# Optimization experiments

Hardware: AMD Instinct MI355X
Metric: run time of the kernel (lower is better)

Reference implementation:

```python
import jax, jax.numpy as jnp
import numpy as np

EPS = 1e-5
HEADS = 8
GROUPS = 8
DIM_HEAD = 64
SCALE = DIM_HEAD ** -0.5
DSF = 4            # downsample_factor
OFF_SCALE = 4.0    # offset_scale
OFF_PAD = 1        # (offset_kernel_size - downsample_factor)//2


def batchnorm(x, g, b):
    # training-mode BatchNorm2d: biased batch stats over (N,H,W)
    m = x.mean(axis=(0, 2, 3), keepdims=True)
    v = x.var(axis=(0, 2, 3), keepdims=True)
    return (x - m) * jax.lax.rsqrt(v + EPS) * g[None, :, None, None] + b[None, :, None, None]


def grouped_conv1x1(x, w):
    # x: (B, G*Ci, H, W), w: (G, Co, Ci) -> (B, G*Co, H, W)
    B, C, H, W = x.shape
    G, Co, Ci = w.shape
    y = jnp.einsum('bgchw,goc->bgohw', x.reshape(B, G, Ci, H, W), w)
    return y.reshape(B, G * Co, H, W)


def conv1x1(x, w, b):
    # x: (B,C,H,W), w: (O,C), b: (O,)
    return jnp.einsum('bchw,oc->bohw', x, w) + b[None, :, None, None]


def norm_grid(h, w):
    # (h,w,2) with channel order (x,y); matches lucidrains create_grid_like+normalize_grid
    # (original normalizes x by h-1, y by w-1; identical for square maps)
    gy, gx = jnp.meshgrid(jnp.arange(h, dtype=jnp.float32), jnp.arange(w, dtype=jnp.float32), indexing='ij')
    nx = 2.0 * gx / max(h - 1, 1) - 1.0
    ny = 2.0 * gy / max(w - 1, 1) - 1.0
    return jnp.stack([nx, ny], axis=-1)


def grid_sample_bilinear(img, grid):
    # img: (N,C,H,W); grid: (N,Hg,Wg,2) with (x,y) in [-1,1]
    # mode='bilinear', padding_mode='zeros', align_corners=False (torch F.grid_sample)
    N, C, H, W = img.shape
    x = ((grid[..., 0] + 1.0) * W - 1.0) * 0.5
    y = ((grid[..., 1] + 1.0) * H - 1.0) * 0.5
    x0 = jnp.floor(x)
    y0 = jnp.floor(y)
    wx1 = x - x0
    wy1 = y - y0
    x0i = x0.astype(jnp.int32)
    y0i = y0.astype(jnp.int32)

    def gather(ix, iy):
        valid = (ix >= 0) & (ix < W) & (iy >= 0) & (iy < H)
        ixc = jnp.clip(ix, 0, W - 1)
        iyc = jnp.clip(iy, 0, H - 1)
        vals = jax.vmap(lambda im, yy, xx: im[:, yy, xx])(img, iyc, ixc)  # (N,C,Hg,Wg)
        return vals * valid[:, None, :, :].astype(img.dtype)

    v00 = gather(x0i, y0i)
    v10 = gather(x0i + 1, y0i)
    v01 = gather(x0i, y0i + 1)
    v11 = gather(x0i + 1, y0i + 1)
    wx1e = wx1[:, None]
    wy1e = wy1[:, None]
    return (v00 * (1 - wx1e) * (1 - wy1e) + v10 * wx1e * (1 - wy1e)
            + v01 * (1 - wx1e) * wy1e + v11 * wx1e * wy1e)


def deformable_attention(x, q_w, k_w, v_w, off_dw_w, off_dw_b, off_pw_w,
                         cpb_w0, cpb_b0, cpb_w1, cpb_b1, cpb_w2, cpb_b2,
                         out_w, out_b):
    B, C, H, W = x.shape
    G = GROUPS
    Cg = C // G  # offset_dims = 64

    q = grouped_conv1x1(x, q_w)  # (B,C,H,W)

    # offsets from grouped queries: depthwise 6x6 stride-4 conv -> GELU -> 1x1 -> tanh*scale
    gq = q.reshape(B * G, Cg, H, W)
    off = jax.lax.conv_general_dilated(
        gq, off_dw_w, window_strides=(DSF, DSF), padding=[(OFF_PAD, OFF_PAD)] * 2,
        feature_group_count=Cg, dimension_numbers=('NCHW', 'OIHW', 'NCHW'))
    off = off + off_dw_b[None, :, None, None]
    off = jax.nn.gelu(off, approximate=False)
    off = jnp.einsum('bchw,oc->bohw', off, off_pw_w)  # (BG,2,h2,w2)
    off = jnp.tanh(off) * OFF_SCALE
    h2, w2 = off.shape[-2:]

    # vgrid = integer grid + offsets, normalized to [-1,1] (channel order x,y)
    gy, gx = jnp.meshgrid(jnp.arange(h2, dtype=x.dtype), jnp.arange(w2, dtype=x.dtype), indexing='ij')
    vgrid = jnp.stack([gx, gy], axis=0)[None] + off  # (BG,2,h2,w2)
    vx = 2.0 * vgrid[:, 0] / max(h2 - 1, 1) - 1.0
    vy = 2.0 * vgrid[:, 1] / max(w2 - 1, 1) - 1.0
    vgrid_scaled = jnp.stack([vx, vy], axis=-1)  # (BG,h2,w2,2)

    # sample kv features at deformed locations
    kv = grid_sample_bilinear(x.reshape(B * G, Cg, H, W), vgrid_scaled)
    kv = kv.reshape(B, C, h2, w2)
    k = grouped_conv1x1(kv, k_w)
    v = grouped_conv1x1(kv, v_w)

    q = q * SCALE

    def to_heads(t):
        b, c, hh, ww = t.shape
        return t.reshape(b, HEADS, DIM_HEAD, hh * ww).transpose(0, 1, 3, 2)  # b h (hw) d

    qh, kh, vh = to_heads(q), to_heads(k), to_heads(v)
    sim = jnp.einsum('bhid,bhjd->bhij', qh, kh)  # (B,H,i=HW,j=h2*w2)

    # continuous positional bias (CPB)
    i, j = H * W, h2 * w2
    grid_q = norm_grid(H, W).reshape(i, 2)
    grid_kv = vgrid_scaled.reshape(B * G, j, 2)
    pos = grid_q[None, :, None, :] - grid_kv[:, None, :, :]  # (BG,i,j,2)
    bias = jnp.sign(pos) * jnp.log(jnp.abs(pos) + 1.0)
    bias = jax.nn.relu(bias @ cpb_w0 + cpb_b0)
    bias = jax.nn.relu(bias @ cpb_w1 + cpb_b1)
    bias = bias @ cpb_w2 + cpb_b2  # (BG,i,j,o) with o = heads//groups = 1
    o = HEADS // G
    bias = bias.reshape(B, G, i, j, o).transpose(0, 1, 4, 2, 3).reshape(B, G * o, i, j)

    attn = jax.nn.softmax(sim + bias, axis=-1)  # (max-subtract in original == stable softmax)
    out = jnp.einsum('bhij,bhjd->bhid', attn, vh)
    out = out.transpose(0, 1, 3, 2).reshape(B, HEADS * DIM_HEAD, H, W)
    return conv1x1(out, out_w, out_b)


def setup_inputs() -> dict:
    key = jax.random.key(0)
    ks = jax.random.split(key, 12)
    B, C, H, W = 2, 512, 32, 32
    G = GROUPS
    s = 0.02
    f32 = jnp.float32
    return {
        'x': jax.random.normal(ks[0], (B, C, H, W), f32),
        'n1_g': jnp.ones((C,), f32), 'n1_b': jnp.zeros((C,), f32),
        'n2_g': jnp.ones((C,), f32), 'n2_b': jnp.zeros((C,), f32),
        'q_w': jax.random.normal(ks[1], (G, C // G, C // G), f32) * s,
        'k_w': jax.random.normal(ks[2], (G, C // G, C // G), f32) * s,
        'v_w': jax.random.normal(ks[3], (G, C // G, C // G), f32) * s,
        'off_dw_w': jax.random.normal(ks[4], (C // G, 1, 6, 6), f32) * s,
        'off_dw_b': jnp.zeros((C // G,), f32),
        'off_pw_w': jax.random.normal(ks[5], (2, C // G), f32) * s,
        'cpb_w0': jax.random.normal(ks[6], (2, 128), f32) * s, 'cpb_b0': jnp.zeros((128,), f32),
        'cpb_w1': jax.random.normal(ks[7], (128, 128), f32) * s, 'cpb_b1': jnp.zeros((128,), f32),
        'cpb_w2': jax.random.normal(ks[8], (128, 1), f32) * s, 'cpb_b2': jnp.zeros((1,), f32),
        'out_w': jax.random.normal(ks[9], (C, C), f32) * s, 'out_b': jnp.zeros((C,), f32),
        'mlp_w1': jax.random.normal(ks[10], (4 * C, C), f32) * s, 'mlp_b1': jnp.zeros((4 * C,), f32),
        'mlp_w2': jax.random.normal(ks[11], (C, 4 * C), f32) * s, 'mlp_b2': jnp.zeros((C,), f32),
    }


def reference(x, n1_g, n1_b, n2_g, n2_b, q_w, k_w, v_w, off_dw_w, off_dw_b, off_pw_w,
              cpb_w0, cpb_b0, cpb_w1, cpb_b1, cpb_w2, cpb_b2, out_w, out_b,
              mlp_w1, mlp_b1, mlp_w2, mlp_b2):
    x = x + deformable_attention(batchnorm(x, n1_g, n1_b), q_w, k_w, v_w,
                                 off_dw_w, off_dw_b, off_pw_w,
                                 cpb_w0, cpb_b0, cpb_w1, cpb_b1, cpb_w2, cpb_b2,
                                 out_w, out_b)
    h = batchnorm(x, n2_g, n2_b)
    h = jax.nn.gelu(conv1x1(h, mlp_w1, mlp_b1), approximate=False)
    h = conv1x1(h, mlp_w2, mlp_b2)
    return x + h
```

## Files before the change

### kernel.cpp

```cpp
#include <hip/hip_runtime.h>
#include <cstdint>
#include <cstddef>

#define BATCH 2
#define CCH   512
#define HWPIX 1024
#define SCALE 0.125f
#define TU0  (-1.45f)
#define TDU  (2.9f/63.0f)
#define TINV (63.0f/2.9f)

typedef short bh8 __attribute__((ext_vector_type(8)));
typedef float f32x4 __attribute__((ext_vector_type(4)));
typedef unsigned short u16;
typedef u16 us8 __attribute__((ext_vector_type(8)));
typedef u16 us4 __attribute__((ext_vector_type(4)));

__device__ __forceinline__ u16 f2bf(float f){
  unsigned u = __float_as_uint(f);
  unsigned r = (u + 0x7FFFu + ((u>>16)&1u))>>16;
  return (u16)r;
}
__device__ __forceinline__ float geluf(float v){ return 0.5f*v*(1.0f + erff(v*0.70710678118654752f)); }

__global__ __launch_bounds__(256) void prep_kernel(
    const float* __restrict__ qw, const float* __restrict__ kw, const float* __restrict__ vw,
    const float* __restrict__ ow, const float* __restrict__ m1, const float* __restrict__ m2,
    u16* __restrict__ wdst,
    const float* __restrict__ x, const float* __restrict__ g, const float* __restrict__ bta,
    float* __restrict__ AB,
    const float* __restrict__ w0, const float* __restrict__ b0,
    const float* __restrict__ w1, const float* __restrict__ b1,
    const float* __restrict__ w2, const float* __restrict__ b2,
    float* __restrict__ tab){
  __shared__ float ls[4], lss[4];
  __shared__ float red[16][17];
  __shared__ __align__(16) float w1s[4096];
  __shared__ float h0s[16*33];
  int blk = blockIdx.x; int t = threadIdx.x;
  if(blk < 2400){
    int idx = (blk*256 + t)*4;
    if(idx >= 2457600) return;
    const float* src; int off;
    if(idx < 32768){ src=qw; off=idx; }
    else if(idx <   65536){ src=kw; off=idx-32768; }
    else if(idx <   98304){ src=vw; off=idx-65536; }
    else if(idx <  360448){ src=ow; off=idx-98304; }
    else if(idx < 1409024){ src=m1; off=idx-360448; }
    else                  { src=m2; off=idx-1409024; }
    float4 v = *(const float4*)&src[off];
    *(us4*)&wdst[idx] = (us4){f2bf(v.x), f2bf(v.y), f2bf(v.z), f2bf(v.w)};
  } else if(blk < 2912){
    int c = blk - 2400;
    float s=0.f, ss=0.f;
    for(int b=0;b<BATCH;b++){
      size_t base = (size_t)b*CCH*HWPIX + (size_t)c*HWPIX;
      for(int p=t;p<HWPIX;p+=256){
        float v = x[base+p];
        s += v; ss += v*v;
      }
    }
    for(int o=32;o;o>>=1){ s += __shfl_down(s,o); ss += __shfl_down(ss,o); }
    int w = t>>6, lane = t&63;
    if(lane==0){ ls[w]=s; lss[w]=ss; }
    __syncthreads();
    if(t==0){
      float S=ls[0]+ls[1]+ls[2]+ls[3], SS=lss[0]+lss[1]+lss[2]+lss[3];
      float m = S*(1.0f/2048.0f);
      float var = SS*(1.0f/2048.0f) - m*m;
      float r = rsqrtf(var + 1e-5f);
      AB[c]     = r*g[c];
      AB[512+c] = bta[c] - m*r*g[c];
    }
  } else {
    int eloc = t & 15, chunk = t >> 4;
    int eb = (blk-2912)*16;
    int e = eb + eloc;
    float acc[8] = {0.f,0.f,0.f,0.f,0.f,0.f,0.f,0.f};
    for(int kc=0;kc<128;kc+=32){
      #pragma unroll
      for(int r=0;r<4;r++){
        int idx = r*1024 + t*4;
        *(f32x4*)&w1s[idx] = *(const f32x4*)&w1[kc*128 + idx];
      }
      #pragma unroll
      for(int j=0;j<2;j++){
        int job = j*256 + t;
        int el = job & 15, kk = job >> 4;
        int ee = eb + el;
        float uu = TU0 + (float)(ee&63)*TDU;
        float vv = TU0 + (float)(ee>>6)*TDU;
        int k = kc + kk;
        h0s[el*33 + kk] = fmaxf(fmaf(uu, w0[k], fmaf(vv, w0[128+k], b0[k])), 0.f);
      }
      __syncthreads();
      #pragma unroll 8
      for(int kk=0;kk<32;kk++){
        float h = h0s[eloc*33 + kk];
        const float* wr = &w1s[kk*128 + chunk*8];
        #pragma unroll
        for(int n=0;n<8;n++) acc[n] = fmaf(h, wr[n], acc[n]);
      }
      __syncthreads();
    }
    float partial = 0.f;
    #pragma unroll
    for(int n=0;n<8;n++)
      partial = fmaf(fmaxf(acc[n] + b1[chunk*8+n], 0.f), w2[chunk*8+n], partial);
    red[eloc][chunk] = partial;
    __syncthreads();
    if(chunk==0){
      float s = b2[0];
      #pragma unroll
      for(int c2=0;c2<16;c2++) s += red[eloc][c2];
      tab[e] = s;
    }
  }
}

__global__ __launch_bounds__(256) void bnstat_kernel(const float* __restrict__ src,
      const float* __restrict__ g, const float* __restrict__ bta, float* __restrict__ AB){
  int c = blockIdx.x; int t = threadIdx.x;
  float s=0.f, ss=0.f;
  for(int b=0;b<BATCH;b++){
    size_t base = (size_t)b*CCH*HWPIX + (size_t)c*HWPIX;
    for(int p=t;p<HWPIX;p+=256){
      float v = src[base+p];
      s += v; ss += v*v;
    }
  }
  for(int o=32;o;o>>=1){ s += __shfl_down(s,o); ss += __shfl_down(ss,o); }
  __shared__ float ls[4], lss[4];
  int w = t>>6, lane = t&63;
  if(lane==0){ ls[w]=s; lss[w]=ss; }
  __syncthreads();
  if(t==0){
    float S=ls[0]+ls[1]+ls[2]+ls[3], SS=lss[0]+lss[1]+lss[2]+lss[3];
    float m = S*(1.0f/2048.0f);
    float var = SS*(1.0f/2048.0f) - m*m;
    float r = rsqrtf(var + 1e-5f);
    AB[c]     = r*g[c];
    AB[512+c] = bta[c] - m*r*g[c];
  }
}

__global__ __launch_bounds__(256) void bntrans_kernel(const float* __restrict__ src,
      const float* __restrict__ AB, float* __restrict__ dstF, u16* __restrict__ dstT, int tMode){
  __shared__ float tile[64*65];
  int t = threadIdx.x;
  int p0 = blockIdx.x*64, gq = blockIdx.y, b = blockIdx.z;
  int pl = t&63, seg = t>>6;
  #pragma unroll
  for(int r=0;r<16;r++){
    int c = seg*16 + r;
    int ch = gq*64 + c;
    size_t a = (size_t)b*524288 + (size_t)ch*1024 + p0 + pl;
    float v = src[a]*AB[ch] + AB[512+ch];
    tile[c*65 + pl] = v;
    if(dstF) dstF[a] = v;
  }
  __syncthreads();
  int c = t&63;
  #pragma unroll
  for(int r=0;r<16;r++){
    int p = seg*16 + r;
    float v = tile[c*65 + p];
    size_t a = tMode ? ((size_t)b*524288 + (size_t)(p0+p)*512 + gq*64 + c)
                     : ((size_t)(b*8+gq)*65536 + (size_t)(p0+p)*64 + c);
    dstT[a] = f2bf(v);
  }
}

template<int NT, int TOUT>
__global__ __launch_bounds__(256,4) void gemm_lds(
    const u16* __restrict__ W, const u16* __restrict__ Xt,
    float* __restrict__ outF, u16* __restrict__ outT,
    const float* __restrict__ bias, const float* __restrict__ resF,
    int M, int K, int Nb, int wMask, int wStride, int doGelu){
  __shared__ __align__(16) u16 xS[64*NT*64];
  __shared__ __align__(16) u16 wS[64*64];
  int t = threadIdx.x;
  int w = t>>6, lane = t&63, l15 = lane&15, quad = lane>>4;
  int n0 = blockIdx.x*(64*NT), m0 = blockIdx.y*64, batch = blockIdx.z;
  const u16* Wg = W + (size_t)(batch & wMask)*wStride + (size_t)m0*K;
  const u16* Xg = Xt + (size_t)batch*Nb*K + (size_t)n0*K;
  const u16* pX[2*NT]; u16* sX[2*NT];
  #pragma unroll
  for(int p=0;p<2*NT;p++){
    int row = (p*256 + t)>>3, kb = t&7;
    pX[p] = Xg + (size_t)row*K + kb*8;
    sX[p] = &xS[(row*8 + (kb ^ (row&7)))*8];
  }
  int row0 = t>>3,        kb0 = t&7;
  int row1 = (256+t)>>3,  kb1 = t&7;
  const u16* pW0 = Wg + (size_t)row0*K + kb0*8;
  const u16* pW1 = Wg + (size_t)row1*K + kb1*8;
  u16* sW0 = &wS[(row0*8 + (kb0 ^ (row0&7)))*8];
  u16* sW1 = &wS[(row1*8 + (kb1 ^ (row1&7)))*8];
  f32x4 acc[4][NT];
  #pragma unroll
  for(int mt=0;mt<4;mt++)
    #pragma unroll
    for(int nt=0;nt<NT;nt++) acc[mt][nt] = (f32x4){0.f,0.f,0.f,0.f};
  us8 rx[2*NT], rw0, rw1;
  #pragma unroll
  for(int p=0;p<2*NT;p++) rx[p] = *(const us8*)pX[p];
  rw0 = *(const us8*)pW0; rw1 = *(const us8*)pW1;
  for(int kc=0;kc<K;kc+=64){
    #pragma unroll
    for(int p=0;p<2*NT;p++) *(us8*)sX[p] = rx[p];
    *(us8*)sW0 = rw0;  *(us8*)sW1 = rw1;
    __syncthreads();
    if(kc+64 < K){
      #pragma unroll
      for(int p=0;p<2*NT;p++) rx[p] = *(const us8*)(pX[p] + kc+64);
      rw0 = *(const us8*)(pW0 + kc+64);  rw1 = *(const us8*)(pW1 + kc+64);
    }
    #pragma unroll
    for(int ks=0;ks<2;ks++){
      bh8 bF[NT];
      #pragma unroll
      for(int nt=0;nt<NT;nt++){
        int rb = (w*NT + nt)*16 + l15;
        bF[nt] = *(const bh8*)&xS[rb*64 + ((ks*4+quad) ^ (rb&7))*8];
      }
      #pragma unroll
      for(int mt=0;mt<4;mt++){
        int ra = mt*16 + l15;
        bh8 aF = *(const bh8*)&wS[ra*64 + ((ks*4+quad) ^ (ra&7))*8];
        #pragma unroll
        for(int nt=0;nt<NT;nt++)
          acc[mt][nt] = __builtin_amdgcn_mfma_f32_16x16x32_bf16(aF, bF[nt], acc[mt][nt], 0,0,0);
      }
    }
    __syncthreads();
  }
  if(TOUT==1){
    size_t oB = (size_t)batch*Nb*(size_t)M;
    #pragma unroll
    for(int nt=0;nt<NT;nt++){
      int n = n0 + (w*NT + nt)*16 + l15;
      #pragma unroll
      for(int mt=0;mt<4;mt++){
        int m = m0 + mt*16 + quad*4;
        us4 pk;
        #pragma unroll
        for(int reg=0;reg<4;reg++){
          float v = acc[mt][nt][reg];
          if(bias) v += bias[m+reg];
          if(doGelu) v = geluf(v);
          pk[reg] = f2bf(v);
        }
        *(us4*)&outT[oB + (size_t)n*M + m] = pk;
      }
    }
  } else if(TOUT==2){
    size_t oBF = (size_t)batch*(size_t)M*Nb;
    size_t oBT = (size_t)batch*Nb*(size_t)M;
    #pragma unroll
    for(int nt=0;nt<NT;nt++){
      int n = n0 + (w*NT + nt)*16 + l15;
      #pragma unroll
      for(int mt=0;mt<4;mt++){
        int m = m0 + mt*16 + quad*4;
        us4 pk;
        #pragma unroll
        for(int reg=0;reg<4;reg++){
          float v = acc[mt][nt][reg];
          outF[oBF + (size_t)(m+reg)*Nb + n] = v;
          pk[reg] = f2bf(v*SCALE);
        }
        *(us4*)&outT[oBT + (size_t)n*M + m] = pk;
      }
    }
  } else {
    size_t oB = (size_t)batch*(size_t)M*Nb;
    #pragma unroll
    for(int nt=0;nt<NT;nt++){
      int n = n0 + (w*NT + nt)*16 + l15;
      #pragma unroll
      for(int mt=0;mt<4;mt++)
        #pragma unroll
        for(int reg=0;reg<4;reg++){
          int m = m0 + mt*16 + quad*4 + reg;
          float v = acc[mt][nt][reg];
          if(bias) v += bias[m];
          if(doGelu) v = geluf(v);
          size_t a = oB + (size_t)m*Nb + n;
          if(resF) v += resF[a];
          outF[a] = v;
        }
    }
  }
}

__global__ __launch_bounds__(256) void dwconv_kernel(const float* __restrict__ q,
    const float* __restrict__ dw, const float* __restrict__ dwb, float* __restrict__ offg){
  int t = threadIdx.x;
  int bgc = blockIdx.x*4 + (t>>6);
  int c = bgc & 63;
  int pix = t&63;
  int oy = pix>>3, ox = pix&7;
  const float* img = q + (size_t)bgc*HWPIX;
  float acc = dwb[c];
  #pragma unroll
  for(int ky=0;ky<6;ky++){
    int y = oy*4 - 1 + ky;
    if(y<0 || y>31) continue;
    #pragma unroll
    for(int kx=0;kx<6;kx++){
      int x = ox*4 - 1 + kx;
      if(x<0 || x>31) continue;
      acc = fmaf(img[y*32 + x], dw[c*36 + ky*6 + kx], acc);
    }
  }
  offg[(size_t)bgc*64 + pix] = geluf(acc);
}

__device__ __forceinline__ float fetchpix(const float* img, int ix, int iy){
  return (ix>=0 && ix<32 && iy>=0 && iy<32) ? img[iy*32+ix] : 0.0f;
}
__global__ __launch_bounds__(256) void samplekv_kernel(
    const float* __restrict__ xn, const float* __restrict__ offg, const float* __restrict__ pw,
    const u16* __restrict__ kwb, const u16* __restrict__ vwb,
    float* __restrict__ vgrid, u16* __restrict__ kTb, float* __restrict__ vbuf){
  __shared__ __align__(16) u16 kvS[64*64];
  __shared__ float redA[64][5], redB[64][5];
  __shared__ float sVG[128];
  int bg = blockIdx.x; int t = threadIdx.x;
  int p = t&63, cq = t>>6;
  float a0=0.f, a1=0.f;
  for(int c=cq*16;c<cq*16+16;c++){
    float v = offg[(size_t)bg*4096 + c*64 + p];
    a0 = fmaf(v, pw[c], a0);
    a1 = fmaf(v, pw[64+c], a1);
  }
  redA[p][cq] = a0; redB[p][cq] = a1;
  __syncthreads();
  if(t < 64){
    float s0 = redA[t][0]+redA[t][1]+redA[t][2]+redA[t][3];
    float s1 = redB[t][0]+redB[t][1]+redB[t][2]+redB[t][3];
    float o0 = tanhf(s0)*4.0f, o1 = tanhf(s1)*4.0f;
    float gx = (float)(t&7), gy = (float)(t>>3);
    float vxx = (2.0f/7.0f)*(gx + o0) - 1.0f;
    float vyy = (2.0f/7.0f)*(gy + o1) - 1.0f;
    sVG[t*2]   = vxx;  sVG[t*2+1] = vyy;
    vgrid[bg*128 + t*2]   = vxx;
    vgrid[bg*128 + t*2+1] = vyy;
  }
  __syncthreads();
  {
    float vx = sVG[p*2], vy = sVG[p*2+1];
    float xs = ((vx + 1.0f)*32.0f - 1.0f)*0.5f;
    float ys = ((vy + 1.0f)*32.0f - 1.0f)*0.5f;
    float x0 = floorf(xs), y0 = floorf(ys);
    float wx = xs - x0, wy = ys - y0;
    int ix0 = (int)x0, iy0 = (int)y0;
    int b = bg>>3, g = bg&7;
    float w00 = (1.f-wx)*(1.f-wy), w10 = wx*(1.f-wy), w01 = (1.f-wx)*wy, w11 = wx*wy;
    u16 tmp[16];
    #pragma unroll
    for(int cc=0;cc<16;cc++){
      int c = cq*16 + cc;
      const float* img = xn + (size_t)b*CCH*HWPIX + (size_t)(g*64+c)*HWPIX;
      float acc = w00*fetchpix(img,ix0,iy0)   + w10*fetchpix(img,ix0+1,iy0)
                + w01*fetchpix(img,ix0,iy0+1) + w11*fetchpix(img,ix0+1,iy0+1);
      tmp[cc] = f2bf(acc);
    }
    int kb0 = cq*2, kb1 = cq*2+1;
    *(us8*)&kvS[p*64 + ((kb0 ^ (p&7))<<3)] = *(us8*)&tmp[0];
    *(us8*)&kvS[p*64 + ((kb1 ^ (p&7))<<3)] = *(us8*)&tmp[8];
  }
  __syncthreads();
  int w = t>>6, lane = t&63, l15 = lane&15, quad = lane>>4;
  int g8 = bg&7;
  const u16* kW = kwb + (size_t)g8*4096 + quad*8;
  const u16* vW = vwb + (size_t)g8*4096 + quad*8;
  int rb = w*16 + l15;
  bh8 bF[2];
  #pragma unroll
  for(int ks=0;ks<2;ks++)
    bF[ks] = *(const bh8*)&kvS[rb*64 + ((ks*4+quad) ^ (rb&7))*8];
  {
    f32x4 acc[4];
    #pragma unroll
    for(int mt=0;mt<4;mt++) acc[mt] = (f32x4){0.f,0.f,0.f,0.f};
    #pragma unroll
    for(int ks=0;ks<2;ks++)
      #pragma unroll
      for(int mt=0;mt<4;mt++){
        bh8 aF = *(const bh8*)&kW[(size_t)(mt*16+l15)*64 + ks*32];
        acc[mt] = __builtin_amdgcn_mfma_f32_16x16x32_bf16(aF, bF[ks], acc[mt], 0,0,0);
      }
    int n = w*16 + l15;
    #pragma unroll
    for(int mt=0;mt<4;mt++){
      us4 pk;
      #pragma unroll
      for(int reg=0;reg<4;reg++) pk[reg] = f2bf(acc[mt][reg]);
      *(us4*)&kTb[(size_t)bg*4096 + (size_t)n*64 + mt*16 + quad*4] = pk;
    }
  }
  {
    f32x4 acc[4];
    #pragma unroll
    for(int mt=0;mt<4;mt++) acc[mt] = (f32x4){0.f,0.f,0.f,0.f};
    #pragma unroll
    for(int ks=0;ks<2;ks++)
      #pragma unroll
      for(int mt=0;mt<4;mt++){
        bh8 aF = *(const bh8*)&vW[(size_t)(mt*16+l15)*64 + ks*32];
        acc[mt] = __builtin_amdgcn_mfma_f32_16x16x32_bf16(aF, bF[ks], acc[mt], 0,0,0);
      }
    int n = w*16 + l15;
    #pragma unroll
    for(int mt=0;mt<4;mt++)
      #pragma unroll
      for(int reg=0;reg<4;reg++)
        vbuf[(size_t)bg*4096 + (size_t)(mt*16 + quad*4 + reg)*64 + n] = acc[mt][reg];
  }
}

__global__ __launch_bounds__(256) void biaseval_kernel(
    const float* __restrict__ vgrid, const float* __restrict__ tab,
    float* __restrict__ biasOut){
  int t = threadIdx.x;
  int bg = blockIdx.x >> 6, jj = blockIdx.x & 63;
  float vx = vgrid[bg*128 + jj*2];
  float vy = vgrid[bg*128 + jj*2 + 1];
  int i0 = t*4;
  int gy = i0 >> 5, gx0 = i0 & 31;
  float py = (2.0f/31.0f)*(float)gy - 1.0f - vy;
  float v = copysignf(__logf(1.0f + fabsf(py)), py);
  float fv = (v - TU0) * TINV;
  int iv = (int)floorf(fv);
  iv = iv < 0 ? 0 : (iv > 62 ? 62 : iv);
  fv -= (float)iv;
  f32x4 res;
  #pragma unroll
  for(int c=0;c<4;c++){
    float px = (2.0f/31.0f)*(float)(gx0 + c) - 1.0f - vx;
    float u = copysignf(__logf(1.0f + fabsf(px)), px);
    float fu = (u - TU0) * TINV;
    int iu = (int)floorf(fu);
    iu = iu < 0 ? 0 : (iu > 62 ? 62 : iu);
    fu -= (float)iu;
    const float* p0 = &tab[iv*64 + iu];
    const float* p1 = p0 + 64;
    float a = fmaf(fu, p0[1] - p0[0], p0[0]);
    float b = fmaf(fu, p1[1] - p1[0], p1[0]);
    res[c] = fmaf(fv, b - a, a);
  }
  *(f32x4*)&biasOut[(size_t)bg*65536 + (size_t)jj*1024 + i0] = res;
}

__global__ __launch_bounds__(256) void attn_kernel(
    const u16* __restrict__ qTb, const u16* __restrict__ kTb, const float* __restrict__ vb,
    const float* __restrict__ biasb, u16* __restrict__ obT){
  __shared__ __align__(16) u16 qS[64*64], kS[64*64];
  __shared__ __align__(16) u16 vS[64*72], pS[64*72];
  int t = threadIdx.x;
  int w = t>>6, lane = t&63, l15 = lane&15, quad = lane>>4;
  int bg = blockIdx.x>>4, itile = blockIdx.x&15;
  int i0 = itile*64;
  #pragma unroll
  for(int p=0;p<2;p++){
    int idx = p*256 + t;
    int row = idx>>3, kb = t&7;
    int sw = ((kb ^ (row&7)))*8;
    *(us8*)&qS[row*64 + sw] = *(const us8*)&qTb[(size_t)bg*65536 + (size_t)(i0+row)*64 + kb*8];
    *(us8*)&kS[row*64 + sw] = *(const us8*)&kTb[(size_t)bg*4096  + (size_t)row*64      + kb*8];
  }
  for(int e=t;e<4096;e+=256){
    int d = e>>6, j = e&63;
    vS[d*72 + j] = f2bf(vb[(size_t)bg*4096 + e]);
  }
  __syncthreads();
  f32x4 sAcc[4];
  #pragma unroll
  for(int jt=0;jt<4;jt++){
    int jg = jt*16 + l15;
    sAcc[jt] = *(const f32x4*)&biasb[(size_t)bg*65536 + (size_t)jg*1024 + i0 + w*16 + quad*4];
  }
  int ra = w*16 + l15;
  #pragma unroll
  for(int ks=0;ks<2;ks++){
    bh8 aF = *(const bh8*)&qS[ra*64 + ((ks*4+quad) ^ (ra&7))*8];
    #pragma unroll
    for(int jt=0;jt<4;jt++){
      int rb = jt*16 + l15;
      bh8 bF = *(const bh8*)&kS[rb*64 + ((ks*4+quad) ^ (rb&7))*8];
      sAcc[jt] = __builtin_amdgcn_mfma_f32_16x16x32_bf16(aF, bF, sAcc[jt], 0,0,0);
    }
  }
  #pragma unroll
  for(int reg=0;reg<4;reg++){
    float m = fmaxf(fmaxf(sAcc[0][reg], sAcc[1][reg]), fmaxf(sAcc[2][reg], sAcc[3][reg]));
    m = fmaxf(m, __shfl_xor(m, 1));
    m = fmaxf(m, __shfl_xor(m, 2));
    m = fmaxf(m, __shfl_xor(m, 4));
    m = fmaxf(m, __shfl_xor(m, 8));
    float li = 0.f;
    #pragma unroll
    for(int jt=0;jt<4;jt++){
      float e = __expf(sAcc[jt][reg] - m);
      sAcc[jt][reg] = e;
      li += e;
    }
    li += __shfl_xor(li, 1);
    li += __shfl_xor(li, 2);
    li += __shfl_xor(li, 4);
    li += __shfl_xor(li, 8);
    float inv = 1.0f / li;
    #pragma unroll
    for(int jt=0;jt<4;jt++) sAcc[jt][reg] *= inv;
  }
  #pragma unroll
  for(int jt=0;jt<4;jt++)
    #pragma unroll
    for(int reg=0;reg<4;reg++)
      pS[(w*16 + quad*4 + reg)*72 + jt*16 + l15] = f2bf(sAcc[jt][reg]);
  __syncthreads();
  f32x4 oAcc[4];
  #pragma unroll
  for(int dt=0;dt<4;dt++) oAcc[dt] = (f32x4){0.f,0.f,0.f,0.f};
  int rp = w*16 + l15;
  #pragma unroll
  for(int ks=0;ks<2;ks++){
    bh8 aP = *(const bh8*)&pS[rp*72 + ks*32 + quad*8];
    #pragma unroll
    for(int dt=0;dt<4;dt++){
      bh8 bV = *(const bh8*)&vS[(dt*16 + l15)*72 + ks*32 + quad*8];
      oAcc[dt] = __builtin_amdgcn_mfma_f32_16x16x32_bf16(aP, bV, oAcc[dt], 0,0,0);
    }
  }
  int b = bg>>3, g = bg&7;
  #pragma unroll
  for(int dt=0;dt<4;dt++)
    #pragma unroll
    for(int reg=0;reg<4;reg++){
      int i = i0 + w*16 + quad*4 + reg;
      obT[(size_t)b*524288 + (size_t)i*512 + g*64 + dt*16 + l15] = f2bf(oAcc[dt][reg]);
    }
}

extern "C" void kernel_launch(void* const* d_in, const int* in_sizes, int n_in,
                              void* d_out, int out_size, void* d_ws, size_t ws_size,
                              hipStream_t stream){
  const float* x    = (const float*)d_in[0];
  const float* n1g  = (const float*)d_in[1];
  const float* n1b  = (const float*)d_in[2];
  const float* n2g  = (const float*)d_in[3];
  const float* n2b  = (const float*)d_in[4];
  const float* qw   = (const float*)d_in[5];
  const float* kw   = (const float*)d_in[6];
  const float* vw   = (const float*)d_in[7];
  const float* dww  = (const float*)d_in[8];
  const float* dwb  = (const float*)d_in[9];
  const float* pww  = (const float*)d_in[10];
  const float* cw0  = (const float*)d_in[11];
  const float* cb0  = (const float*)d_in[12];
  const float* cw1  = (const float*)d_in[13];
  const float* cb1  = (const float*)d_in[14];
  const float* cw2  = (const float*)d_in[15];
  const float* cb2  = (const float*)d_in[16];
  const float* ow   = (const float*)d_in[17];
  const float* obb  = (const float*)d_in[18];
  const float* m1w  = (const float*)d_in[19];
  const float* m1bi = (const float*)d_in[20];
  const float* m2w  = (const float*)d_in[21];
  const float* m2bi = (const float*)d_in[22];
  float* out = (float*)d_out;
  float* ws = (float*)d_ws;

  float* xn     = ws;
  float* x2     = ws + 1048576;
  float* q      = ws + 2097152;
  float* biasb  = ws + 3145728;
  u16*   hT     = (u16*)(ws + 2097152);
  u16*   attnT  = (u16*)(ws + 4194304);
  u16*   xnT    = (u16*)(ws + 4718592);
  float* tab    = ws + 5242880;
  u16*   kTb    = (u16*)(ws + 5275648);
  float* vbuf   = ws + 5341184;
  float* offg   = ws + 5406720;
  float* bnAB   = offg;
  float* vgrid  = ws + 5472256;
  u16*   wbf    = (u16*)(ws + 5474304);
  u16*   qTb    = (u16*)(ws + 6703104);
  u16 *qwb = wbf, *kwb = wbf+32768, *vwb = wbf+65536, *owb = wbf+98304;
  u16 *m1wb = wbf+360448, *m2wb = wbf+1409024;

  prep_kernel<<<3168,256,0,stream>>>(qw,kw,vw,ow,m1w,m2w,wbf,
                                     x,n1g,n1b,bnAB,
                                     cw0,cb0,cw1,cb1,cw2,cb2,tab);
  bntrans_kernel<<<dim3(16,8,2),256,0,stream>>>(x, bnAB, xn, xnT, 0);
  gemm_lds<1,2><<<dim3(16,1,16),256,0,stream>>>(qwb, xnT, q, qTb, nullptr, nullptr,
                                                64,64,1024, 7, 4096, 0);
  dwconv_kernel<<<256,256,0,stream>>>(q, dww, dwb, offg);
  samplekv_kernel<<<16,256,0,stream>>>(xn, offg, pww, kwb, vwb, vgrid, kTb, vbuf);
  biaseval_kernel<<<1024,256,0,stream>>>(vgrid, tab, biasb);
  attn_kernel<<<256,256,0,stream>>>(qTb, kTb, vbuf, biasb, attnT);
  gemm_lds<1,0><<<dim3(16,8,2),256,0,stream>>>(owb, attnT, x2, nullptr, obb, x,
                                               512,512,1024, 0,0,0);
  bnstat_kernel<<<512,256,0,stream>>>(x2, n2g, n2b, bnAB);
  bntrans_kernel<<<dim3(16,8,2),256,0,stream>>>(x2, bnAB, nullptr, xnT, 1);
  gemm_lds<2,1><<<dim3(8,32,2),256,0,stream>>>(m1wb, xnT, nullptr, hT, m1bi, nullptr,
                                               2048,512,1024, 0,0,1);
  gemm_lds<1,0><<<dim3(16,8,2),256,0,stream>>>(m2wb, hT, out, nullptr, m2bi, x2,
                                               512,2048,1024, 0,0,0);
}
```

Measured before the change: 211.9 us.

## Fuse bias evaluation into attention and BN2 stats into output-projection GEMM

Removes the separate relative-position bias kernel: the attention kernel now computes the log-spaced bias from the table for each score element, which avoids writing and reading a large bias buffer. Also removes the BN2 statistics kernel: the output-projection GEMM epilogue reduces sums and squared sums across lanes and accumulates them with atomics into a stats buffer that dwconv zeroes. A new transpose kernel derives the scale and shift from those stats. In exchange, the attention kernel does more transcendental math, the atomics are contended, and float-atomic summation order is nondeterministic.

```diff
diff --git a/kernel.cpp b/kernel.cpp
--- a/kernel.cpp
+++ b/kernel.cpp
@@ -118,34 +118,8 @@
   }
 }
 
-__global__ __launch_bounds__(256) void bnstat_kernel(const float* __restrict__ src,
-      const float* __restrict__ g, const float* __restrict__ bta, float* __restrict__ AB){
-  int c = blockIdx.x; int t = threadIdx.x;
-  float s=0.f, ss=0.f;
-  for(int b=0;b<BATCH;b++){
-    size_t base = (size_t)b*CCH*HWPIX + (size_t)c*HWPIX;
-    for(int p=t;p<HWPIX;p+=256){
-      float v = src[base+p];
-      s += v; ss += v*v;
-    }
-  }
-  for(int o=32;o;o>>=1){ s += __shfl_down(s,o); ss += __shfl_down(ss,o); }
-  __shared__ float ls[4], lss[4];
-  int w = t>>6, lane = t&63;
-  if(lane==0){ ls[w]=s; lss[w]=ss; }
-  __syncthreads();
-  if(t==0){
-    float S=ls[0]+ls[1]+ls[2]+ls[3], SS=lss[0]+lss[1]+lss[2]+lss[3];
-    float m = S*(1.0f/2048.0f);
-    float var = SS*(1.0f/2048.0f) - m*m;
-    float r = rsqrtf(var + 1e-5f);
-    AB[c]     = r*g[c];
-    AB[512+c] = bta[c] - m*r*g[c];
-  }
-}
-
 __global__ __launch_bounds__(256) void bntrans_kernel(const float* __restrict__ src,
-      const float* __restrict__ AB, float* __restrict__ dstF, u16* __restrict__ dstT, int tMode){
+      const float* __restrict__ AB, float* __restrict__ dstF, u16* __restrict__ dstT){
   __shared__ float tile[64*65];
   int t = threadIdx.x;
   int p0 = blockIdx.x*64, gq = blockIdx.y, b = blockIdx.z;
@@ -157,7 +131,7 @@
     size_t a = (size_t)b*524288 + (size_t)ch*1024 + p0 + pl;
     float v = src[a]*AB[ch] + AB[512+ch];
     tile[c*65 + pl] = v;
-    if(dstF) dstF[a] = v;
+    dstF[a] = v;
   }
   __syncthreads();
   int c = t&63;
@@ -165,17 +139,49 @@
   for(int r=0;r<16;r++){
     int p = seg*16 + r;
     float v = tile[c*65 + p];
-    size_t a = tMode ? ((size_t)b*524288 + (size_t)(p0+p)*512 + gq*64 + c)
-                     : ((size_t)(b*8+gq)*65536 + (size_t)(p0+p)*64 + c);
-    dstT[a] = f2bf(v);
-  }
-}
-
-template<int NT, int TOUT>
+    dstT[(size_t)(b*8+gq)*65536 + (size_t)(p0+p)*64 + c] = f2bf(v);
+  }
+}
+
+__global__ __launch_bounds__(256) void bntrans2_kernel(const float* __restrict__ src,
+      const float* __restrict__ stats, const float* __restrict__ g, const float* __restrict__ bta,
+      u16* __restrict__ dstT){
+  __shared__ float tile[64*65];
+  __shared__ float sA[64], sB[64];
+  int t = threadIdx.x;
+  int p0 = blockIdx.x*64, gq = blockIdx.y, b = blockIdx.z;
+  if(t < 64){
+    int ch = gq*64 + t;
+    float s = stats[ch], ss = stats[512+ch];
+    float m = s*(1.0f/2048.0f);
+    float var = ss*(1.0f/2048.0f) - m*m;
+    float r = rsqrtf(var + 1e-5f);
+    sA[t] = r*g[ch];
+    sB[t] = bta[ch] - m*r*g[ch];
+  }
+  __syncthreads();
+  int pl = t&63, seg = t>>6;
+  #pragma unroll
+  for(int r=0;r<16;r++){
+    int c = seg*16 + r;
+    size_t a = (size_t)b*524288 + (size_t)(gq*64+c)*1024 + p0 + pl;
+    tile[c*65 + pl] = src[a]*sA[c] + sB[c];
+  }
+  __syncthreads();
+  int c = t&63;
+  #pragma unroll
+  for(int r=0;r<16;r++){
+    int p = seg*16 + r;
+    dstT[(size_t)b*524288 + (size_t)(p0+p)*512 + gq*64 + c] = f2bf(tile[c*65 + p]);
+  }
+}
+
+template<int NT, int TOUT, int ST>
 __global__ __launch_bounds__(256,4) void gemm_lds(
     const u16* __restrict__ W, const u16* __restrict__ Xt,
     float* __restrict__ outF, u16* __restrict__ outT,
     const float* __restrict__ bias, const float* __restrict__ resF,
+    float* __restrict__ stats,
     int M, int K, int Nb, int wMask, int wStride, int doGelu){
   __shared__ __align__(16) u16 xS[64*NT*64];
   __shared__ __align__(16) u16 wS[64*64];
@@ -289,14 +295,28 @@
           size_t a = oB + (size_t)m*Nb + n;
           if(resF) v += resF[a];
           outF[a] = v;
+          if(ST){
+            float sv = v, sv2 = v*v;
+            sv += __shfl_xor(sv, 1);  sv2 += __shfl_xor(sv2, 1);
+            sv += __shfl_xor(sv, 2);  sv2 += __shfl_xor(sv2, 2);
+            sv += __shfl_xor(sv, 4);  sv2 += __shfl_xor(sv2, 4);
+            sv += __shfl_xor(sv, 8);  sv2 += __shfl_xor(sv2, 8);
+            if(l15==0){
+              atomicAdd(&stats[m], sv);
+              atomicAdd(&stats[512+m], sv2);
+            }
+          }
         }
     }
   }
 }
 
 __global__ __launch_bounds__(256) void dwconv_kernel(const float* __restrict__ q,
-    const float* __restrict__ dw, const float* __restrict__ dwb, float* __restrict__ offg){
+    const float* __restrict__ dw, const float* __restrict__ dwb, float* __restrict__ offg,
+    float* __restrict__ stats){
   int t = threadIdx.x;
+  if(blockIdx.x == 0)
+    *(f32x4*)&stats[t*4] = (f32x4){0.f,0.f,0.f,0.f};
   int bgc = blockIdx.x*4 + (t>>6);
   int c = bgc & 63;
   int pix = t&63;
@@ -421,48 +441,17 @@
   }
 }
 
-__global__ __launch_bounds__(256) void biaseval_kernel(
-    const float* __restrict__ vgrid, const float* __restrict__ tab,
-    float* __restrict__ biasOut){
-  int t = threadIdx.x;
-  int bg = blockIdx.x >> 6, jj = blockIdx.x & 63;
-  float vx = vgrid[bg*128 + jj*2];
-  float vy = vgrid[bg*128 + jj*2 + 1];
-  int i0 = t*4;
-  int gy = i0 >> 5, gx0 = i0 & 31;
-  float py = (2.0f/31.0f)*(float)gy - 1.0f - vy;
-  float v = copysignf(__logf(1.0f + fabsf(py)), py);
-  float fv = (v - TU0) * TINV;
-  int iv = (int)floorf(fv);
-  iv = iv < 0 ? 0 : (iv > 62 ? 62 : iv);
-  fv -= (float)iv;
-  f32x4 res;
-  #pragma unroll
-  for(int c=0;c<4;c++){
-    float px = (2.0f/31.0f)*(float)(gx0 + c) - 1.0f - vx;
-    float u = copysignf(__logf(1.0f + fabsf(px)), px);
-    float fu = (u - TU0) * TINV;
-    int iu = (int)floorf(fu);
-    iu = iu < 0 ? 0 : (iu > 62 ? 62 : iu);
-    fu -= (float)iu;
-    const float* p0 = &tab[iv*64 + iu];
-    const float* p1 = p0 + 64;
-    float a = fmaf(fu, p0[1] - p0[0], p0[0]);
-    float b = fmaf(fu, p1[1] - p1[0], p1[0]);
-    res[c] = fmaf(fv, b - a, a);
-  }
-  *(f32x4*)&biasOut[(size_t)bg*65536 + (size_t)jj*1024 + i0] = res;
-}
-
 __global__ __launch_bounds__(256) void attn_kernel(
     const u16* __restrict__ qTb, const u16* __restrict__ kTb, const float* __restrict__ vb,
-    const float* __restrict__ biasb, u16* __restrict__ obT){
+    const float* __restrict__ vgrid, const float* __restrict__ tab, u16* __restrict__ obT){
   __shared__ __align__(16) u16 qS[64*64], kS[64*64];
   __shared__ __align__(16) u16 vS[64*72], pS[64*72];
+  __shared__ float sVG[128];
   int t = threadIdx.x;
   int w = t>>6, lane = t&63, l15 = lane&15, quad = lane>>4;
   int bg = blockIdx.x>>4, itile = blockIdx.x&15;
   int i0 = itile*64;
+  if(t < 128) sVG[t] = vgrid[bg*128 + t];
   #pragma unroll
   for(int p=0;p<2;p++){
     int idx = p*256 + t;
@@ -476,11 +465,34 @@
     vS[d*72 + j] = f2bf(vb[(size_t)bg*4096 + e]);
   }
   __syncthreads();
+  int iBase = i0 + w*16 + quad*4;
+  float qy = (2.0f/31.0f)*(float)(iBase>>5) - 1.0f;
+  float qx0 = (float)(iBase&31);
   f32x4 sAcc[4];
   #pragma unroll
   for(int jt=0;jt<4;jt++){
-    int jg = jt*16 + l15;
-    sAcc[jt] = *(const f32x4*)&biasb[(size_t)bg*65536 + (size_t)jg*1024 + i0 + w*16 + quad*4];
+    int j = jt*16 + l15;
+    float vx = sVG[j*2], vy = sVG[j*2+1];
+    float py = qy - vy;
+    float v = copysignf(__logf(1.0f + fabsf(py)), py);
+    float fv = (v - TU0) * TINV;
+    int iv = (int)floorf(fv);
+    iv = iv < 0 ? 0 : (iv > 62 ? 62 : iv);
+    fv -= (float)iv;
+    #pragma unroll
+    for(int reg=0;reg<4;reg++){
+      float px = (2.0f/31.0f)*(qx0 + (float)reg) - 1.0f - vx;
+      float u = copysignf(__logf(1.0f + fabsf(px)), px);
+      float fu = (u - TU0) * TINV;
+      int iu = (int)floorf(fu);
+      iu = iu < 0 ? 0 : (iu > 62 ? 62 : iu);
+      fu -= (float)iu;
+      const float* p0 = &tab[iv*64 + iu];
+      const float* p1 = p0 + 64;
+      float a = fmaf(fu, p0[1] - p0[0], p0[0]);
+      float b = fmaf(fu, p1[1] - p1[0], p1[0]);
+      sAcc[jt][reg] = fmaf(fv, b - a, a);
+    }
   }
   int ra = w*16 + l15;
   #pragma unroll
@@ -576,7 +588,6 @@
   float* xn     = ws;
   float* x2     = ws + 1048576;
   float* q      = ws + 2097152;
-  float* biasb  = ws + 3145728;
   u16*   hT     = (u16*)(ws + 2097152);
   u16*   attnT  = (u16*)(ws + 4194304);
   u16*   xnT    = (u16*)(ws + 4718592);
@@ -588,25 +599,24 @@
   float* vgrid  = ws + 5472256;
   u16*   wbf    = (u16*)(ws + 5474304);
   u16*   qTb    = (u16*)(ws + 6703104);
+  float* stats  = ws + 7340032;
   u16 *qwb = wbf, *kwb = wbf+32768, *vwb = wbf+65536, *owb = wbf+98304;
   u16 *m1wb = wbf+360448, *m2wb = wbf+1409024;
 
   prep_kernel<<<3168,256,0,stream>>>(qw,kw,vw,ow,m1w,m2w,wbf,
                                      x,n1g,n1b,bnAB,
                                      cw0,cb0,cw1,cb1,cw2,cb2,tab);
-  bntrans_kernel<<<dim3(16,8,2),256,0,stream>>>(x, bnAB, xn, xnT, 0);
-  gemm_lds<1,2><<<dim3(16,1,16),256,0,stream>>>(qwb, xnT, q, qTb, nullptr, nullptr,
-                                                64,64,1024, 7, 4096, 0);
-  dwconv_kernel<<<256,256,0,stream>>>(q, dww, dwb, offg);
+  bntrans_kernel<<<dim3(16,8,2),256,0,stream>>>(x, bnAB, xn, xnT);
+  gemm_lds<1,2,0><<<dim3(16,1,16),256,0,stream>>>(qwb, xnT, q, qTb, nullptr, nullptr, nullptr,
+                                                  64,64,1024, 7, 4096, 0);
+  dwconv_kernel<<<256,256,0,stream>>>(q, dww, dwb, offg, stats);
   samplekv_kernel<<<16,256,0,stream>>>(xn, offg, pww, kwb, vwb, vgrid, kTb, vbuf);
-  biaseval_kernel<<<1024,256,0,stream>>>(vgrid, tab, biasb);
-  attn_kernel<<<256,256,0,stream>>>(qTb, kTb, vbuf, biasb, attnT);
-  gemm_lds<1,0><<<dim3(16,8,2),256,0,stream>>>(owb, attnT, x2, nullptr, obb, x,
-                                               512,512,1024, 0,0,0);
-  bnstat_kernel<<<512,256,0,stream>>>(x2, n2g, n2b, bnAB);
-  bntrans_kernel<<<dim3(16,8,2),256,0,stream>>>(x2, bnAB, nullptr, xnT, 1);
-  gemm_lds<2,1><<<dim3(8,32,2),256,0,stream>>>(m1wb, xnT, nullptr, hT, m1bi, nullptr,
-                                               2048,512,1024, 0,0,1);
-  gemm_lds<1,0><<<dim3(16,8,2),256,0,stream>>>(m2wb, hT, out, nullptr, m2bi, x2,
-                                               512,2048,1024, 0,0,0);
-}
+  attn_kernel<<<256,256,0,stream>>>(qTb, kTb, vbuf, vgrid, tab, attnT);
+  gemm_lds<1,0,1><<<dim3(16,8,2),256,0,stream>>>(owb, attnT, x2, nullptr, obb, x, stats,
+                                                 512,512,1024, 0,0,0);
+  bntrans2_kernel<<<dim3(16,8,2),256,0,stream>>>(x2, stats, n2g, n2b, xnT);
+  gemm_lds<2,1,0><<<dim3(8,32,2),256,0,stream>>>(m1wb, xnT, nullptr, hT, m1bi, nullptr, nullptr,
+                                                 2048,512,1024, 0,0,1);
+  gemm_lds<1,0,0><<<dim3(16,8,2),256,0,stream>>>(m2wb, hT, out, nullptr, m2bi, x2, nullptr,
+                                                 512,2048,1024, 0,0,0);
+}
```

Measured after the change: 213.9 us. Within noise of the previous version (+0.9%).
